# Optimization experiments

Measured on AMD Instinct MI355X. Metric: run time of the kernel, lower is better.

## Reference

```python
import jax, jax.numpy as jnp
import numpy as np

B, L, D = 8, 2048, 1024

def setup_inputs() -> dict:
    key = jax.random.key(0)
    ks = jax.random.split(key, 4)
    s = 1.0 / np.sqrt(D)  # linear init scale
    x = jax.random.normal(ks[0], (B, L, D), dtype=jnp.float32)
    mask = jnp.zeros((B, L, L), dtype=jnp.float32)  # additive attention mask
    Wq = jax.random.normal(ks[1], (D, D), dtype=jnp.float32) * s
    Wk = jax.random.normal(ks[2], (D, D), dtype=jnp.float32) * s
    Wv = jax.random.normal(ks[3], (D, D), dtype=jnp.float32) * s
    bq = jnp.zeros((D,), dtype=jnp.float32)
    bk = jnp.zeros((D,), dtype=jnp.float32)
    bv = jnp.zeros((D,), dtype=jnp.float32)
    return {"x": x, "mask": mask, "Wq": Wq, "bq": bq, "Wk": Wk, "bk": bk, "Wv": Wv, "bv": bv}

def reference(x, mask, Wq, bq, Wk, bk, Wv, bv):
    # Linear projections (torch Linear: y = x @ W.T + b)
    q = jnp.einsum('bld,ed->ble', x, Wq) + bq
    k = jnp.einsum('bld,ed->ble', x, Wk) + bk
    v = jnp.einsum('bld,ed->ble', x, Wv) + bv
    d = x.shape[2]
    logits = jnp.einsum('bqd,bkd->bqk', q, k) / jnp.sqrt(jnp.float32(d))
    probas = jax.nn.softmax(logits + mask, axis=2)
    return jnp.einsum('bqk,bkd->bqd', probas, v)
```

## Files before the change

kernel.cpp:

```cpp
#include <hip/hip_runtime.h>
#include <hip/hip_bf16.h>

typedef __attribute__((ext_vector_type(8))) short short8;
typedef __attribute__((ext_vector_type(4))) float floatx4;

__device__ __forceinline__ unsigned short f2bf(float f) {
    unsigned int u = __builtin_bit_cast(unsigned int, f);
    u += 0x7fffu + ((u >> 16) & 1u);
    return (unsigned short)(u >> 16);
}

__device__ __forceinline__ void gl_lds16(const unsigned short* g, unsigned short* l) {
    __builtin_amdgcn_global_load_lds(
        (const __attribute__((address_space(1))) unsigned int*)(const void*)g,
        (__attribute__((address_space(3))) unsigned int*)(void*)l,
        16, 0, 0);
}

#define BM 128
#define BN 128
#define BK 64

template<bool OUT_BF16>
__global__ void gemm_bt(const unsigned short* __restrict__ A,
                        const unsigned short* __restrict__ B,
                        void* __restrict__ O, const float* __restrict__ bias,
                        int bias_mode, int K, int lda, int ldb, int ldo,
                        long long aBS, long long bBS, long long oBS,
                        float scale, int nbx)
{
    __shared__ __align__(16) unsigned short As[BM * BK];
    __shared__ __align__(16) unsigned short Bs[BN * BK];

    const int t = threadIdx.x;
    const int z = blockIdx.z;

    const int nwg = gridDim.x;
    const int cpx = nwg >> 3;
    const int swz = (blockIdx.x & 7) * cpx + (blockIdx.x >> 3);
    const int bx = swz % nbx, by = swz / nbx;
    const size_t m0 = (size_t)bx * BM;
    const size_t n0 = (size_t)by * BN;

    const unsigned short* Az = A + (size_t)z * aBS;
    const unsigned short* Bz = B + (size_t)z * bBS;

    const int lane = t & 63;
    const int w = t >> 6;
    const int lq = lane >> 4, lr = lane & 15;
    const int wr = w >> 1, wc = w & 1;

    const int srow = t >> 3;
    const int scol = (t & 7) * 8;
    unsigned short* lA = As + w * 512;
    unsigned short* lB = Bs + w * 512;

    floatx4 acc[4][4];
#pragma unroll
    for (int i = 0; i < 4; ++i)
#pragma unroll
        for (int j = 0; j < 4; ++j)
            acc[i][j] = (floatx4){0.f, 0.f, 0.f, 0.f};

    for (int kt = 0; kt < K; kt += BK) {
        const unsigned short* ga = Az + (m0 + srow) * (size_t)lda + kt + scol;
        const unsigned short* gb = Bz + (n0 + srow) * (size_t)ldb + kt + scol;
#pragma unroll
        for (int s = 0; s < 4; ++s) {
            gl_lds16(ga + (size_t)s * 32 * lda, lA + s * 2048);
            gl_lds16(gb + (size_t)s * 32 * ldb, lB + s * 2048);
        }
        __syncthreads();
#pragma unroll
        for (int kk = 0; kk < 2; ++kk) {
            short8 af[4], bf[4];
#pragma unroll
            for (int mi = 0; mi < 4; ++mi)
                af[mi] = *(const short8*)&As[(wr * 64 + mi * 16 + lr) * BK + kk * 32 + lq * 8];
#pragma unroll
            for (int ni = 0; ni < 4; ++ni)
                bf[ni] = *(const short8*)&Bs[(wc * 64 + ni * 16 + lr) * BK + kk * 32 + lq * 8];
#pragma unroll
            for (int mi = 0; mi < 4; ++mi)
#pragma unroll
                for (int ni = 0; ni < 4; ++ni)
                    acc[mi][ni] = __builtin_amdgcn_mfma_f32_16x16x32_bf16(af[mi], bf[ni], acc[mi][ni], 0, 0, 0);
        }
        __syncthreads();
    }

#pragma unroll
    for (int mi = 0; mi < 4; ++mi) {
#pragma unroll
        for (int ni = 0; ni < 4; ++ni) {
            const size_t col = n0 + wc * 64 + ni * 16 + lr;
            const float cb = (bias_mode == 1) ? bias[col] : 0.f;
            floatx4 v = acc[mi][ni];
#pragma unroll
            for (int r = 0; r < 4; ++r) {
                const size_t row = m0 + wr * 64 + mi * 16 + lq * 4 + r;
                float val = v[r] * scale + cb;
                if (bias_mode == 2) val += bias[row];
                if (OUT_BF16)
                    ((unsigned short*)O)[(size_t)z * oBS + row * (size_t)ldo + col] = f2bf(val);
                else
                    ((float*)O)[(size_t)z * oBS + row * (size_t)ldo + col] = val;
            }
        }
    }
}

__global__ void cvt_f2b(const float4* __restrict__ src, ushort4* __restrict__ dst, int n4)
{
    int i = blockIdx.x * blockDim.x + threadIdx.x;
    const int stride = gridDim.x * blockDim.x;
    for (; i < n4; i += stride) {
        float4 f = src[i];
        dst[i] = (ushort4){f2bf(f.x), f2bf(f.y), f2bf(f.z), f2bf(f.w)};
    }
}

__global__ void softmax_kernel(float* __restrict__ S, const float* __restrict__ mask, int b0)
{
    const int lane = threadIdx.x & 63;
    const int wid = threadIdx.x >> 6;
    const size_t rowid = (size_t)blockIdx.x * 4 + wid;
    const size_t bi = rowid >> 11;
    const size_t q = rowid & 2047;
    float* Srow = S + rowid * 2048;
    const float* Mrow = mask + (((size_t)b0 + bi) * 2048 + q) * 2048;

    float4 v[8];
    float mx = -3.4e38f;
#pragma unroll
    for (int i = 0; i < 8; ++i) {
        float4 s = ((const float4*)Srow)[i * 64 + lane];
        float4 m = ((const float4*)Mrow)[i * 64 + lane];
        s.x += m.x; s.y += m.y; s.z += m.z; s.w += m.w;
        v[i] = s;
        mx = fmaxf(mx, fmaxf(fmaxf(s.x, s.y), fmaxf(s.z, s.w)));
    }
#pragma unroll
    for (int off = 32; off; off >>= 1) mx = fmaxf(mx, __shfl_xor(mx, off, 64));
    float sum = 0.f;
#pragma unroll
    for (int i = 0; i < 8; ++i) {
        v[i].x = __expf(v[i].x - mx);
        v[i].y = __expf(v[i].y - mx);
        v[i].z = __expf(v[i].z - mx);
        v[i].w = __expf(v[i].w - mx);
        sum += v[i].x + v[i].y + v[i].z + v[i].w;
    }
#pragma unroll
    for (int off = 32; off; off >>= 1) sum += __shfl_xor(sum, off, 64);
    const float inv = 1.0f / sum;

    unsigned short* Prow = (unsigned short*)Srow;
#pragma unroll
    for (int i = 0; i < 8; ++i) {
        ushort4 h = {f2bf(v[i].x * inv), f2bf(v[i].y * inv),
                     f2bf(v[i].z * inv), f2bf(v[i].w * inv)};
        ((ushort4*)Prow)[i * 64 + lane] = h;
    }
}

extern "C" void kernel_launch(void* const* d_in, const int* in_sizes, int n_in,
                              void* d_out, int out_size, void* d_ws, size_t ws_size,
                              hipStream_t stream)
{
    const float* x    = (const float*)d_in[0];
    const float* mask = (const float*)d_in[1];
    const float* Wq   = (const float*)d_in[2];
    const float* bq   = (const float*)d_in[3];
    const float* Wk   = (const float*)d_in[4];
    const float* bk   = (const float*)d_in[5];
    const float* Wv   = (const float*)d_in[6];
    const float* bv   = (const float*)d_in[7];
    float* out = (float*)d_out;

    const size_t MB = 1ull << 20;
    char* ws = (char*)d_ws;
    unsigned short* Qb  = (unsigned short*)(ws);
    unsigned short* Kb  = (unsigned short*)(ws + 32 * MB);
    unsigned short* Vt  = (unsigned short*)(ws + 64 * MB);
    unsigned short* Wqb = (unsigned short*)(ws + 96 * MB);
    unsigned short* Wkb = (unsigned short*)(ws + 98 * MB);
    unsigned short* Wvb = (unsigned short*)(ws + 100 * MB);
    unsigned short* xb  = (unsigned short*)(ws + 102 * MB);
    float* Sb = (float*)(ws + 102 * MB);

    size_t savail = (ws_size > 102 * MB) ? ws_size - 102 * MB : 0;
    int g = 1;
    if (savail >= 128 * MB) g = 8;
    else if (savail >= 64 * MB) g = 4;
    else if (savail >= 32 * MB) g = 2;

    dim3 blk(256, 1, 1);

    cvt_f2b<<<2048, 256, 0, stream>>>((const float4*)x, (ushort4*)xb, 16384 * 1024 / 4);
    cvt_f2b<<<512, 256, 0, stream>>>((const float4*)Wq, (ushort4*)Wqb, 1024 * 1024 / 4);
    cvt_f2b<<<512, 256, 0, stream>>>((const float4*)Wk, (ushort4*)Wkb, 1024 * 1024 / 4);
    cvt_f2b<<<512, 256, 0, stream>>>((const float4*)Wv, (ushort4*)Wvb, 1024 * 1024 / 4);

    gemm_bt<true><<<dim3(128 * 8, 1, 1), blk, 0, stream>>>(
        xb, Wqb, Qb, bq, 1, 1024, 1024, 1024, 1024, 0LL, 0LL, 0LL, 1.0f, 128);
    gemm_bt<true><<<dim3(128 * 8, 1, 1), blk, 0, stream>>>(
        xb, Wkb, Kb, bk, 1, 1024, 1024, 1024, 1024, 0LL, 0LL, 0LL, 1.0f, 128);
    gemm_bt<true><<<dim3(8 * 128, 1, 1), blk, 0, stream>>>(
        Wvb, xb, Vt, bv, 2, 1024, 1024, 1024, 16384, 0LL, 0LL, 0LL, 1.0f, 8);

    const float sscale = 0.03125f;
    for (int b0 = 0; b0 < 8; b0 += g) {
        const int gb = (8 - b0 < g) ? (8 - b0) : g;
        gemm_bt<false><<<dim3(256, 1, gb), blk, 0, stream>>>(
            Qb + (size_t)b0 * 2048 * 1024, Kb + (size_t)b0 * 2048 * 1024, Sb,
            (const float*)nullptr, 0, 1024, 1024, 1024, 2048,
            2048LL * 1024, 2048LL * 1024, 2048LL * 2048, sscale, 16);
        softmax_kernel<<<dim3(gb * 512, 1, 1), blk, 0, stream>>>(Sb, mask, b0);
        gemm_bt<false><<<dim3(128, 1, gb), blk, 0, stream>>>(
            (const unsigned short*)Sb, Vt + (size_t)b0 * 2048,
            out + (size_t)b0 * 2048 * 1024, (const float*)nullptr, 0,
            2048, 4096, 16384, 1024,
            2048LL * 4096, 2048LL, 2048LL * 1024, 1.0f, 16);
    }
}
```

Measured before the change: 611.2 us.

## Rewrite GEMM as 256x256 tile, 8-wave, double-buffered LDS pipeline with swizzle

The bf16 GEMM kernel moves from 128x128 tiles with 4 waves to 256x256 tiles with 8 waves. It adds double-buffered LDS with global_load_lds prefetch of the next K tiles, interleaved across four MFMA phases with explicit vmcnt waits and barriers. LDS columns are XOR-swizzled to avoid bank conflicts, and setprio is raised around MFMA bursts. The goal is to hide global load latency and raise MFMA utilisation. The cost is much higher register and LDS pressure and fewer workgroups per GEMM, down to 32 per batch for the PV GEMM, which may underfill the GPU.

```diff
diff --git a/kernel.cpp b/kernel.cpp
--- a/kernel.cpp
+++ b/kernel.cpp
@@ -17,80 +17,125 @@
         16, 0, 0);
 }
 
-#define BM 128
-#define BN 128
+#define BM 256
+#define BN 256
 #define BK 64
 
 template<bool OUT_BF16>
-__global__ void gemm_bt(const unsigned short* __restrict__ A,
-                        const unsigned short* __restrict__ B,
-                        void* __restrict__ O, const float* __restrict__ bias,
-                        int bias_mode, int K, int lda, int ldb, int ldo,
-                        long long aBS, long long bBS, long long oBS,
-                        float scale, int nbx)
-{
-    __shared__ __align__(16) unsigned short As[BM * BK];
-    __shared__ __align__(16) unsigned short Bs[BN * BK];
+__global__ __launch_bounds__(512, 2)
+void gemm_bt(const unsigned short* __restrict__ A,
+             const unsigned short* __restrict__ B,
+             void* __restrict__ O, const float* __restrict__ bias,
+             int bias_mode, int K, int lda, int ldb, int ldo,
+             long long aBS, long long bBS, long long oBS,
+             float scale, int nby)
+{
+    __shared__ __align__(16) unsigned short lds[2][2][BM * BK];
 
     const int t = threadIdx.x;
+    const int lane = t & 63;
+    const int w = t >> 6;
+    const int wr = w >> 2;
+    const int wc = w & 3;
+    const int lq = lane >> 4;
+    const int lr = lane & 15;
+
+    const int nwg = gridDim.x;
+    const int swz = (blockIdx.x & 7) * (nwg >> 3) + (blockIdx.x >> 3);
+    const int by = swz % nby, bx = swz / nby;
+    const size_t m0 = (size_t)bx * BM, n0 = (size_t)by * BN;
+
     const int z = blockIdx.z;
-
-    const int nwg = gridDim.x;
-    const int cpx = nwg >> 3;
-    const int swz = (blockIdx.x & 7) * cpx + (blockIdx.x >> 3);
-    const int bx = swz % nbx, by = swz / nbx;
-    const size_t m0 = (size_t)bx * BM;
-    const size_t n0 = (size_t)by * BN;
-
     const unsigned short* Az = A + (size_t)z * aBS;
     const unsigned short* Bz = B + (size_t)z * bBS;
 
-    const int lane = t & 63;
-    const int w = t >> 6;
-    const int lq = lane >> 4, lr = lane & 15;
-    const int wr = w >> 1, wc = w & 1;
-
     const int srow = t >> 3;
-    const int scol = (t & 7) * 8;
-    unsigned short* lA = As + w * 512;
-    unsigned short* lB = Bs + w * 512;
-
-    floatx4 acc[4][4];
-#pragma unroll
-    for (int i = 0; i < 4; ++i)
+    const int scol = ((t & 7) ^ (srow & 7)) << 3;
+
+    floatx4 acc[8][4];
+#pragma unroll
+    for (int i = 0; i < 8; ++i)
 #pragma unroll
         for (int j = 0; j < 4; ++j)
             acc[i][j] = (floatx4){0.f, 0.f, 0.f, 0.f};
 
-    for (int kt = 0; kt < K; kt += BK) {
-        const unsigned short* ga = Az + (m0 + srow) * (size_t)lda + kt + scol;
-        const unsigned short* gb = Bz + (n0 + srow) * (size_t)ldb + kt + scol;
-#pragma unroll
-        for (int s = 0; s < 4; ++s) {
-            gl_lds16(ga + (size_t)s * 32 * lda, lA + s * 2048);
-            gl_lds16(gb + (size_t)s * 32 * ldb, lB + s * 2048);
+    const int NT = K / BK;
+
+    auto stage = [&](int mat, int u, int kt, int buf) {
+        const unsigned short* g = (mat ? Bz + (n0 + u * 64 + srow) * (size_t)ldb
+                                       : Az + (m0 + u * 64 + srow) * (size_t)lda) + kt + scol;
+        gl_lds16(g, &lds[buf][mat][u * 4096 + w * 512]);
+    };
+
+#pragma unroll
+    for (int u = 0; u < 4; ++u) stage(1, u, 0, 0);
+#pragma unroll
+    for (int u = 0; u < 4; ++u) stage(0, u, 0, 0);
+    if (NT > 1) {
+#pragma unroll
+        for (int u = 0; u < 4; ++u) stage(1, u, BK, 1);
+        asm volatile("s_waitcnt vmcnt(4)" ::: "memory");
+    } else {
+        asm volatile("s_waitcnt vmcnt(0)" ::: "memory");
+    }
+    __builtin_amdgcn_s_barrier();
+    __builtin_amdgcn_sched_barrier(0);
+
+    for (int tt = 0; tt < NT; ++tt) {
+        const int cur = tt & 1, nxt = cur ^ 1;
+        const int kt1 = (tt + 1) * BK, kt2 = (tt + 2) * BK;
+        short8 bfr[4][2];
+#pragma unroll
+        for (int p = 0; p < 4; ++p) {
+            short8 af[2][2];
+            if (p == 0) {
+#pragma unroll
+                for (int ni = 0; ni < 4; ++ni)
+#pragma unroll
+                    for (int kk = 0; kk < 2; ++kk) {
+                        const int rb = wc * 64 + ni * 16 + lr;
+                        const int j = kk * 4 + lq;
+                        bfr[ni][kk] = *(const short8*)&lds[cur][1][rb * 64 + ((j ^ (rb & 7)) << 3)];
+                    }
+            }
+#pragma unroll
+            for (int mi2 = 0; mi2 < 2; ++mi2)
+#pragma unroll
+                for (int kk = 0; kk < 2; ++kk) {
+                    const int ra = wr * 128 + (2 * p + mi2) * 16 + lr;
+                    const int j = kk * 4 + lq;
+                    af[mi2][kk] = *(const short8*)&lds[cur][0][ra * 64 + ((j ^ (ra & 7)) << 3)];
+                }
+            if (p == 0 && tt + 1 < NT) { stage(0, 0, kt1, nxt); stage(0, 1, kt1, nxt); }
+            if (p == 1 && tt + 1 < NT) { stage(0, 2, kt1, nxt); stage(0, 3, kt1, nxt); }
+            if (p == 2 && tt + 2 < NT) { stage(1, 0, kt2, cur); stage(1, 1, kt2, cur); }
+            if (p == 3 && tt + 2 < NT) { stage(1, 2, kt2, cur); stage(1, 3, kt2, cur); }
+
+            __builtin_amdgcn_sched_barrier(0);
+            __builtin_amdgcn_s_barrier();
+            __builtin_amdgcn_sched_barrier(0);
+            __builtin_amdgcn_s_setprio(1);
+#pragma unroll
+            for (int kk = 0; kk < 2; ++kk)
+#pragma unroll
+                for (int mi2 = 0; mi2 < 2; ++mi2)
+#pragma unroll
+                    for (int ni = 0; ni < 4; ++ni)
+                        acc[2 * p + mi2][ni] = __builtin_amdgcn_mfma_f32_16x16x32_bf16(
+                            af[mi2][kk], bfr[ni][kk], acc[2 * p + mi2][ni], 0, 0, 0);
+            __builtin_amdgcn_s_setprio(0);
+            __builtin_amdgcn_sched_barrier(0);
+            if (p == 3) {
+                if (tt < NT - 2) asm volatile("s_waitcnt vmcnt(4)" ::: "memory");
+                else             asm volatile("s_waitcnt vmcnt(0)" ::: "memory");
+            }
+            __builtin_amdgcn_s_barrier();
+            __builtin_amdgcn_sched_barrier(0);
         }
-        __syncthreads();
-#pragma unroll
-        for (int kk = 0; kk < 2; ++kk) {
-            short8 af[4], bf[4];
-#pragma unroll
-            for (int mi = 0; mi < 4; ++mi)
-                af[mi] = *(const short8*)&As[(wr * 64 + mi * 16 + lr) * BK + kk * 32 + lq * 8];
-#pragma unroll
-            for (int ni = 0; ni < 4; ++ni)
-                bf[ni] = *(const short8*)&Bs[(wc * 64 + ni * 16 + lr) * BK + kk * 32 + lq * 8];
-#pragma unroll
-            for (int mi = 0; mi < 4; ++mi)
-#pragma unroll
-                for (int ni = 0; ni < 4; ++ni)
-                    acc[mi][ni] = __builtin_amdgcn_mfma_f32_16x16x32_bf16(af[mi], bf[ni], acc[mi][ni], 0, 0, 0);
-        }
-        __syncthreads();
-    }
-
-#pragma unroll
-    for (int mi = 0; mi < 4; ++mi) {
+    }
+
+#pragma unroll
+    for (int mi = 0; mi < 8; ++mi) {
 #pragma unroll
         for (int ni = 0; ni < 4; ++ni) {
             const size_t col = n0 + wc * 64 + ni * 16 + lr;
@@ -98,7 +143,7 @@
             floatx4 v = acc[mi][ni];
 #pragma unroll
             for (int r = 0; r < 4; ++r) {
-                const size_t row = m0 + wr * 64 + mi * 16 + lq * 4 + r;
+                const size_t row = m0 + wr * 128 + mi * 16 + lq * 4 + r;
                 float val = v[r] * scale + cb;
                 if (bias_mode == 2) val += bias[row];
                 if (OUT_BF16)
@@ -195,32 +240,32 @@
     else if (savail >= 64 * MB) g = 4;
     else if (savail >= 32 * MB) g = 2;
 
-    dim3 blk(256, 1, 1);
+    dim3 blk(512, 1, 1);
 
     cvt_f2b<<<2048, 256, 0, stream>>>((const float4*)x, (ushort4*)xb, 16384 * 1024 / 4);
     cvt_f2b<<<512, 256, 0, stream>>>((const float4*)Wq, (ushort4*)Wqb, 1024 * 1024 / 4);
     cvt_f2b<<<512, 256, 0, stream>>>((const float4*)Wk, (ushort4*)Wkb, 1024 * 1024 / 4);
     cvt_f2b<<<512, 256, 0, stream>>>((const float4*)Wv, (ushort4*)Wvb, 1024 * 1024 / 4);
 
-    gemm_bt<true><<<dim3(128 * 8, 1, 1), blk, 0, stream>>>(
-        xb, Wqb, Qb, bq, 1, 1024, 1024, 1024, 1024, 0LL, 0LL, 0LL, 1.0f, 128);
-    gemm_bt<true><<<dim3(128 * 8, 1, 1), blk, 0, stream>>>(
-        xb, Wkb, Kb, bk, 1, 1024, 1024, 1024, 1024, 0LL, 0LL, 0LL, 1.0f, 128);
-    gemm_bt<true><<<dim3(8 * 128, 1, 1), blk, 0, stream>>>(
-        Wvb, xb, Vt, bv, 2, 1024, 1024, 1024, 16384, 0LL, 0LL, 0LL, 1.0f, 8);
+    gemm_bt<true><<<dim3(256, 1, 1), blk, 0, stream>>>(
+        xb, Wqb, Qb, bq, 1, 1024, 1024, 1024, 1024, 0LL, 0LL, 0LL, 1.0f, 4);
+    gemm_bt<true><<<dim3(256, 1, 1), blk, 0, stream>>>(
+        xb, Wkb, Kb, bk, 1, 1024, 1024, 1024, 1024, 0LL, 0LL, 0LL, 1.0f, 4);
+    gemm_bt<true><<<dim3(256, 1, 1), blk, 0, stream>>>(
+        Wvb, xb, Vt, bv, 2, 1024, 1024, 1024, 16384, 0LL, 0LL, 0LL, 1.0f, 64);
 
     const float sscale = 0.03125f;
     for (int b0 = 0; b0 < 8; b0 += g) {
         const int gb = (8 - b0 < g) ? (8 - b0) : g;
-        gemm_bt<false><<<dim3(256, 1, gb), blk, 0, stream>>>(
+        gemm_bt<false><<<dim3(64, 1, gb), blk, 0, stream>>>(
             Qb + (size_t)b0 * 2048 * 1024, Kb + (size_t)b0 * 2048 * 1024, Sb,
             (const float*)nullptr, 0, 1024, 1024, 1024, 2048,
-            2048LL * 1024, 2048LL * 1024, 2048LL * 2048, sscale, 16);
-        softmax_kernel<<<dim3(gb * 512, 1, 1), blk, 0, stream>>>(Sb, mask, b0);
-        gemm_bt<false><<<dim3(128, 1, gb), blk, 0, stream>>>(
+            2048LL * 1024, 2048LL * 1024, 2048LL * 2048, sscale, 8);
+        softmax_kernel<<<dim3(gb * 512, 1, 1), dim3(256), 0, stream>>>(Sb, mask, b0);
+        gemm_bt<false><<<dim3(32, 1, gb), blk, 0, stream>>>(
             (const unsigned short*)Sb, Vt + (size_t)b0 * 2048,
             out + (size_t)b0 * 2048 * 1024, (const float*)nullptr, 0,
             2048, 4096, 16384, 1024,
-            2048LL * 4096, 2048LL, 2048LL * 1024, 1.0f, 16);
-    }
-}
+            2048LL * 4096, 2048LL, 2048LL * 1024, 1.0f, 4);
+    }
+}
```

After: 557.0 us. -8.9%, faster.
